# Kernel optimization log

Measured on AMD Instinct MI355X. Metric: run time of the kernel, lower is better.

The kernel has to match this reference:

```python
import jax, jax.numpy as jnp
import numpy as np

N_NODES = 100000
N_EDGES = 1600000
EMBED_DIM = 128
HIDDEN_DIM = 256


def setup_inputs() -> dict:
    key = jax.random.key(0)
    k_emb, k_src, k_dst, k_w1, k_w2 = jax.random.split(key, 5)
    emb = jax.random.normal(k_emb, (N_NODES, EMBED_DIM), dtype=jnp.float32)
    edge_src = jax.random.randint(k_src, (N_EDGES,), 0, N_NODES)
    edge_dst = jax.random.randint(k_dst, (N_EDGES,), 0, N_NODES)
    # Linear(2D -> H) and Linear(H -> D), stored as [in, out] for x @ W
    W1 = jax.random.normal(k_w1, (2 * EMBED_DIM, HIDDEN_DIM), dtype=jnp.float32) * (1.0 / np.sqrt(2 * EMBED_DIM))
    b1 = jnp.zeros((HIDDEN_DIM,), dtype=jnp.float32)
    W2 = jax.random.normal(k_w2, (HIDDEN_DIM, EMBED_DIM), dtype=jnp.float32) * (1.0 / np.sqrt(HIDDEN_DIM))
    b2 = jnp.zeros((EMBED_DIM,), dtype=jnp.float32)
    return {"emb": emb, "edge_src": edge_src, "edge_dst": edge_dst,
            "W1": W1, "b1": b1, "W2": W2, "b2": b2}


def reference(emb, edge_src, edge_dst, W1, b1, W2, b2):
    N, D = emb.shape
    E = edge_src.shape[0]
    # gather neighbor embeddings and segment-mean per destination node
    gathered = emb[edge_src]                                    # [E, D]
    nbr_sum = jax.ops.segment_sum(gathered, edge_dst, num_segments=N)   # [N, D]
    counts = jax.ops.segment_sum(jnp.ones((E,), emb.dtype), edge_dst, num_segments=N)  # [N]
    nbr_mean = nbr_sum / jnp.maximum(counts, 1.0)[:, None]
    # nodes with no neighbors fall back to their own embedding
    nbr_mean = jnp.where(counts[:, None] == 0, emb, nbr_mean)
    concat = jnp.concatenate([emb, nbr_mean], axis=-1)          # [N, 2D]
    h = jax.nn.relu(concat @ W1 + b1)                           # [N, H]
    return h @ W2 + b2                                          # [N, D]
```

## Files before the change

### kernel.cpp

```cpp
#include <hip/hip_runtime.h>

#define DD 128
#define HH 256
#define K1 256
#define BM 64
#define CH 2048
#define CH1 4096
#define CAP 8192

typedef __bf16 bf16;
typedef __attribute__((ext_vector_type(8))) __bf16 bf16x8;
typedef __attribute__((ext_vector_type(4))) float f32x4;


__global__ __launch_bounds__(256) void count512_k(const int* __restrict__ dst,
                                                  int* __restrict__ bcnt,
                                                  int E, int BSH) {
    __shared__ int c[512];
    for (int j = threadIdx.x; j < 512; j += 256) c[j] = 0;
    __syncthreads();
    for (int e = blockIdx.x * 256 + threadIdx.x; e < E; e += gridDim.x * 256)
        atomicAdd(&c[dst[e] >> BSH], 1);
    __syncthreads();
    for (int j = threadIdx.x; j < 512; j += 256)
        if (c[j]) atomicAdd(&bcnt[j], c[j]);
}

__global__ __launch_bounds__(512) void scan512_k(const int* __restrict__ bcnt,
                                                 int* __restrict__ bbase,
                                                 int* __restrict__ bpos,
                                                 int NB, int E) {
    __shared__ int s[512];
    const int t = threadIdx.x;
    int v = (t < NB) ? bcnt[t] : 0;
    s[t] = v;
    __syncthreads();
    for (int off = 1; off < 512; off <<= 1) {
        int y = (t >= off) ? s[t - off] : 0;
        __syncthreads();
        s[t] += y;
        __syncthreads();
    }
    int excl = s[t] - v;
    if (t < NB) { bbase[t] = excl; bpos[t] = excl; }
    if (t == 0) bbase[NB] = E;
}

__global__ __launch_bounds__(256) void part512_k(const int* __restrict__ src,
                                                 const int* __restrict__ dst,
                                                 int* __restrict__ bpos,
                                                 int2* __restrict__ pairs,
                                                 int E, int BSH) {
    __shared__ int lcnt[512];
    __shared__ int lbase[512];
    const int t = threadIdx.x;
    const int e0 = blockIdx.x * CH1;
    const int e1 = min(E, e0 + CH1);
    for (int j = t; j < 512; j += 256) lcnt[j] = 0;
    __syncthreads();
    int rs[CH1 / 256];
    #pragma unroll
    for (int k = 0; k < CH1 / 256; ++k) {
        int e = e0 + k * 256 + t;
        int b = -1;
        if (e < e1) { b = dst[e] >> BSH; atomicAdd(&lcnt[b], 1); }
        rs[k] = b;
    }
    __syncthreads();
    for (int j = t; j < 512; j += 256) {
        int c = lcnt[j];
        lbase[j] = c ? atomicAdd(&bpos[j], c) : 0;
        lcnt[j] = 0;
    }
    __syncthreads();
    #pragma unroll
    for (int k = 0; k < CH1 / 256; ++k) {
        int e = e0 + k * 256 + t;
        if (e < e1) {
            int b = rs[k];
            int slot = lbase[b] + atomicAdd(&lcnt[b], 1);
            pairs[slot] = make_int2(src[e], dst[e]);
        }
    }
}

__global__ __launch_bounds__(256) void sortb_k(const int2* __restrict__ pairs,
                                               const int* __restrict__ bbase,
                                               int* __restrict__ offs,
                                               int* __restrict__ ssrc,
                                               int N, int BSH) {
    __shared__ int hist[512];
    __shared__ int pref[512];
    __shared__ int run[512];
    __shared__ int sorted[CAP];
    const int t = threadIdx.x;
    const int b = blockIdx.x;
    const int B = 1 << BSH;
    const int d0 = b << BSH;
    const int nd = min(B, N - d0);
    const int rb = bbase[b], re = bbase[b + 1];
    const int cntE = re - rb;
    for (int j = t; j < 512; j += 256) hist[j] = 0;
    __syncthreads();
    for (int i = rb + t; i < re; i += 256)
        atomicAdd(&hist[pairs[i].y - d0], 1);
    __syncthreads();
    for (int j = t; j < 512; j += 256) pref[j] = hist[j];
    __syncthreads();
    for (int off = 1; off < 512; off <<= 1) {
        int j2 = t + 256;
        int v0 = (t >= off) ? pref[t - off] : 0;
        int v1 = (j2 >= off) ? pref[j2 - off] : 0;
        __syncthreads();
        pref[t] += v0;
        pref[j2] += v1;
        __syncthreads();
    }
    for (int j = t; j < nd; j += 256) offs[d0 + j] = rb + pref[j];
    for (int j = t; j < 512; j += 256) run[j] = pref[j] - hist[j];
    __syncthreads();
    if (cntE <= CAP) {
        for (int i = rb + t; i < re; i += 256) {
            int2 p = pairs[i];
            int pos = atomicAdd(&run[p.y - d0], 1);
            sorted[pos] = p.x;
        }
        __syncthreads();
        for (int i = t; i < cntE; i += 256) ssrc[rb + i] = sorted[i];
    } else {
        for (int i = rb + t; i < re; i += 256) {
            int2 p = pairs[i];
            int pos = atomicAdd(&run[p.y - d0], 1);
            ssrc[rb + pos] = p.x;
        }
    }
}


__global__ __launch_bounds__(256) void hist_k(const int* __restrict__ dst,
                                              int* __restrict__ cnt, int E) {
    for (int e = blockIdx.x * blockDim.x + threadIdx.x; e < E;
         e += gridDim.x * blockDim.x)
        atomicAdd(&cnt[dst[e]], 1);
}

__global__ __launch_bounds__(256) void scan1_k(const int* __restrict__ cnt,
                                               int* __restrict__ offs,
                                               int* __restrict__ part, int N) {
    __shared__ int sdata[256];
    const int b = blockIdx.x, t = threadIdx.x;
    const int base = b * 1024 + t * 4;
    int v[4], sum = 0;
    #pragma unroll
    for (int i = 0; i < 4; ++i) {
        int idx = base + i;
        v[i] = (idx < N) ? cnt[idx] : 0;
        sum += v[i];
    }
    sdata[t] = sum;
    __syncthreads();
    for (int off = 1; off < 256; off <<= 1) {
        int y = (t >= off) ? sdata[t - off] : 0;
        __syncthreads();
        sdata[t] += y;
        __syncthreads();
    }
    int excl = sdata[t] - sum;
    if (t == 255) part[b] = sdata[255];
    int run = excl;
    #pragma unroll
    for (int i = 0; i < 4; ++i) {
        int idx = base + i;
        if (idx < N) offs[idx] = run;
        run += v[i];
    }
}

__global__ __launch_bounds__(128) void scan2_k(int* __restrict__ part, int nparts) {
    __shared__ int sdata[128];
    const int t = threadIdx.x;
    int v = (t < nparts) ? part[t] : 0;
    sdata[t] = v;
    __syncthreads();
    for (int off = 1; off < 128; off <<= 1) {
        int y = (t >= off) ? sdata[t - off] : 0;
        __syncthreads();
        sdata[t] += y;
        __syncthreads();
    }
    if (t < nparts) part[t] = sdata[t] - v;
}

__global__ __launch_bounds__(256) void scan3_k(int* __restrict__ offs,
                                               const int* __restrict__ part, int N) {
    for (int i = blockIdx.x * blockDim.x + threadIdx.x; i < N;
         i += gridDim.x * blockDim.x)
        offs[i] += part[i >> 10];
}

__global__ __launch_bounds__(256) void bucket_k(const int* __restrict__ src,
                                                const int* __restrict__ dst,
                                                int* __restrict__ offs,
                                                int* __restrict__ ssrc,
                                                int E, int N) {
    const int r = blockIdx.x & 7;
    const int chunk = blockIdx.x >> 3;
    const int lo = r * (N >> 3);
    const int hi = (r == 7) ? N : lo + (N >> 3);
    const int e0 = chunk * CH;
    const int e1 = min(E, e0 + CH);
    for (int e = e0 + threadIdx.x; e < e1; e += 256) {
        int d = dst[e];
        if (d >= lo && d < hi) {
            int pos = atomicAdd(&offs[d], 1);
            ssrc[pos] = src[e];
        }
    }
}

__global__ __launch_bounds__(256) void cvt_k(const float* __restrict__ emb,
                                             bf16* __restrict__ embh, size_t n8) {
    for (size_t i = blockIdx.x * blockDim.x + threadIdx.x; i < n8;
         i += (size_t)gridDim.x * blockDim.x) {
        float4 a = *reinterpret_cast<const float4*>(&emb[i * 8]);
        float4 b = *reinterpret_cast<const float4*>(&emb[i * 8 + 4]);
        bf16x8 v;
        v[0]=(bf16)a.x; v[1]=(bf16)a.y; v[2]=(bf16)a.z; v[3]=(bf16)a.w;
        v[4]=(bf16)b.x; v[5]=(bf16)b.y; v[6]=(bf16)b.z; v[7]=(bf16)b.w;
        *reinterpret_cast<bf16x8*>(&embh[i * 8]) = v;
    }
}

__global__ __launch_bounds__(256) void gather_bf16_k(const bf16* __restrict__ embh,
                                                     const int* __restrict__ offs,
                                                     const int* __restrict__ ssrc,
                                                     bf16* __restrict__ nbrh, int N) {
    const int wid = threadIdx.x >> 6;
    const int lane = threadIdx.x & 63;
    const int d = blockIdx.x * 4 + wid;
    if (d >= N) return;
    const int sub = lane >> 4;
    const int c8 = (lane & 15) * 8;
    const int start = (d == 0) ? 0 : offs[d - 1];
    const int end = offs[d];
    float acc[8];
    #pragma unroll
    for (int j = 0; j < 8; ++j) acc[j] = 0.f;
    int e = start;
    for (; e + 8 <= end; e += 8) {
        int s0 = ssrc[e + sub];
        int s1 = ssrc[e + 4 + sub];
        bf16x8 v0 = *reinterpret_cast<const bf16x8*>(&embh[(size_t)s0 * DD + c8]);
        bf16x8 v1 = *reinterpret_cast<const bf16x8*>(&embh[(size_t)s1 * DD + c8]);
        #pragma unroll
        for (int j = 0; j < 8; ++j) acc[j] += (float)v0[j] + (float)v1[j];
    }
    for (; e + 4 <= end; e += 4) {
        int s = ssrc[e + sub];
        bf16x8 v = *reinterpret_cast<const bf16x8*>(&embh[(size_t)s * DD + c8]);
        #pragma unroll
        for (int j = 0; j < 8; ++j) acc[j] += (float)v[j];
    }
    const int rem = end - e;
    if (sub < rem) {
        int s = ssrc[e + sub];
        bf16x8 v = *reinterpret_cast<const bf16x8*>(&embh[(size_t)s * DD + c8]);
        #pragma unroll
        for (int j = 0; j < 8; ++j) acc[j] += (float)v[j];
    }
    #pragma unroll
    for (int j = 0; j < 8; ++j) {
        acc[j] += __shfl_xor(acc[j], 16);
        acc[j] += __shfl_xor(acc[j], 32);
    }
    if (sub == 0) {
        bf16x8 o;
        if (end > start) {
            float inv = 1.f / (float)(end - start);
            #pragma unroll
            for (int j = 0; j < 8; ++j) o[j] = (bf16)(acc[j] * inv);
        } else {
            o = *reinterpret_cast<const bf16x8*>(&embh[(size_t)d * DD + c8]);
        }
        *reinterpret_cast<bf16x8*>(&nbrh[(size_t)d * DD + c8]) = o;
    }
}

__global__ __launch_bounds__(256) void gather_k(const float* __restrict__ emb,
                                                const int* __restrict__ offs,
                                                const int* __restrict__ ssrc,
                                                float* __restrict__ nbr, int N) {
    const int wid = threadIdx.x >> 6;
    const int lane = threadIdx.x & 63;
    const int d = blockIdx.x * 4 + wid;
    if (d >= N) return;
    const int sub = lane >> 5;
    const int c = (lane & 31) * 4;
    const int start = (d == 0) ? 0 : offs[d - 1];
    const int end = offs[d];
    float4 acc = make_float4(0.f, 0.f, 0.f, 0.f);
    int e = start;
    for (; e + 4 <= end; e += 4) {
        int s0 = ssrc[e + sub];
        int s1 = ssrc[e + 2 + sub];
        float4 v0 = *reinterpret_cast<const float4*>(&emb[(size_t)s0 * DD + c]);
        float4 v1 = *reinterpret_cast<const float4*>(&emb[(size_t)s1 * DD + c]);
        acc.x += v0.x + v1.x; acc.y += v0.y + v1.y;
        acc.z += v0.z + v1.z; acc.w += v0.w + v1.w;
    }
    for (; e + 2 <= end; e += 2) {
        int s = ssrc[e + sub];
        float4 v = *reinterpret_cast<const float4*>(&emb[(size_t)s * DD + c]);
        acc.x += v.x; acc.y += v.y; acc.z += v.z; acc.w += v.w;
    }
    if (e < end && sub == 0) {
        int s = ssrc[e];
        float4 v = *reinterpret_cast<const float4*>(&emb[(size_t)s * DD + c]);
        acc.x += v.x; acc.y += v.y; acc.z += v.z; acc.w += v.w;
    }
    acc.x += __shfl_xor(acc.x, 32);
    acc.y += __shfl_xor(acc.y, 32);
    acc.z += __shfl_xor(acc.z, 32);
    acc.w += __shfl_xor(acc.w, 32);
    if (sub == 0) {
        if (end > start) {
            float inv = 1.f / (float)(end - start);
            acc.x *= inv; acc.y *= inv; acc.z *= inv; acc.w *= inv;
        } else {
            acc = *reinterpret_cast<const float4*>(&emb[(size_t)d * DD + c]);
        }
        *reinterpret_cast<float4*>(&nbr[(size_t)d * DD + c]) = acc;
    }
}

__global__ __launch_bounds__(64) void pack_k(const float* __restrict__ W, int NC,
                                             bf16* __restrict__ hi) {
    const int ntiles = NC >> 4;
    const int kt = blockIdx.x / ntiles;
    const int nt = blockIdx.x % ntiles;
    const int l = threadIdx.x;
    const int k0 = kt * 32 + (l >> 4) * 8;
    const int n = nt * 16 + (l & 15);
    bf16x8 hv;
    #pragma unroll
    for (int r = 0; r < 8; ++r)
        hv[r] = (bf16)W[(size_t)(k0 + r) * NC + n];
    *reinterpret_cast<bf16x8*>(hi + ((size_t)blockIdx.x * 64 + l) * 8) = hv;
}

__global__ __launch_bounds__(256) void mlp_mfma_k(const float* __restrict__ emb,
        const bf16* __restrict__ embh,
        const float* nbrf, const bf16* __restrict__ nbrh,
        const bf16* __restrict__ w1h, const float* __restrict__ b1,
        const bf16* __restrict__ w2h, const float* __restrict__ b2,
        float* out, int N) {
    __shared__ char smem[BM * K1 * 2];
    const int t = threadIdx.x;
    const int n0 = blockIdx.x * BM;
    const int l = t & 63;
    const int w = t >> 6;

    #pragma unroll
    for (int i = 0; i < 8; ++i) {
        int chunk = i * 256 + t;
        int row = chunk >> 5;
        int c0 = (chunk & 31) * 8;
        int n = n0 + row;
        bf16x8 hv;
        if (n < N) {
            if (embh != nullptr) {
                const bf16* sp = (c0 < DD) ? &embh[(size_t)n * DD + c0]
                                           : &nbrh[(size_t)n * DD + (c0 - DD)];
                hv = *reinterpret_cast<const bf16x8*>(sp);
            } else {
                const float* sp = (c0 < DD) ? &emb[(size_t)n * DD + c0]
                                            : &nbrf[(size_t)n * DD + (c0 - DD)];
                float4 a = *reinterpret_cast<const float4*>(sp);
                float4 b = *reinterpret_cast<const float4*>(sp + 4);
                hv[0]=(bf16)a.x; hv[1]=(bf16)a.y; hv[2]=(bf16)a.z; hv[3]=(bf16)a.w;
                hv[4]=(bf16)b.x; hv[5]=(bf16)b.y; hv[6]=(bf16)b.z; hv[7]=(bf16)b.w;
            }
        } else {
            #pragma unroll
            for (int j = 0; j < 8; ++j) hv[j] = (bf16)0.f;
        }
        int off = row * 512 + ((c0 * 2) ^ ((row & 7) << 4));
        *reinterpret_cast<bf16x8*>(smem + off) = hv;
    }
    __syncthreads();

    const int arow = l & 15;
    const int abyte = (l >> 4) * 16;

    f32x4 acc[4][4];
    #pragma unroll
    for (int ntl = 0; ntl < 4; ++ntl) {
        float bv = b1[w * 64 + ntl * 16 + (l & 15)];
        #pragma unroll
        for (int mt = 0; mt < 4; ++mt)
            acc[mt][ntl] = (f32x4){bv, bv, bv, bv};
    }
    for (int kt = 0; kt < 8; ++kt) {
        bf16x8 ah[4];
        #pragma unroll
        for (int mt = 0; mt < 4; ++mt) {
            int row = mt * 16 + arow;
            int off = row * 512 + ((kt * 64 + abyte) ^ ((row & 7) << 4));
            ah[mt] = *reinterpret_cast<const bf16x8*>(smem + off);
        }
        #pragma unroll
        for (int ntl = 0; ntl < 4; ++ntl) {
            int nt = w * 4 + ntl;
            size_t boff = ((size_t)(kt * 16 + nt) * 64 + l) * 8;
            bf16x8 bh = *reinterpret_cast<const bf16x8*>(w1h + boff);
            #pragma unroll
            for (int mt = 0; mt < 4; ++mt)
                acc[mt][ntl] = __builtin_amdgcn_mfma_f32_16x16x32_bf16(ah[mt], bh, acc[mt][ntl], 0, 0, 0);
        }
    }
    __syncthreads();

    #pragma unroll
    for (int mt = 0; mt < 4; ++mt)
        #pragma unroll
        for (int ntl = 0; ntl < 4; ++ntl) {
            int col = w * 64 + ntl * 16 + (l & 15);
            #pragma unroll
            for (int r = 0; r < 4; ++r) {
                int row = mt * 16 + (l >> 4) * 4 + r;
                int off = row * 512 + ((col * 2) ^ ((row & 7) << 4));
                *reinterpret_cast<bf16*>(smem + off) = (bf16)fmaxf(acc[mt][ntl][r], 0.f);
            }
        }
    __syncthreads();

    f32x4 acc2[4][2];
    #pragma unroll
    for (int ntl = 0; ntl < 2; ++ntl) {
        float bv = b2[w * 32 + ntl * 16 + (l & 15)];
        #pragma unroll
        for (int mt = 0; mt < 4; ++mt)
            acc2[mt][ntl] = (f32x4){bv, bv, bv, bv};
    }
    for (int kt = 0; kt < 8; ++kt) {
        bf16x8 ah[4];
        #pragma unroll
        for (int mt = 0; mt < 4; ++mt) {
            int row = mt * 16 + arow;
            int off = row * 512 + ((kt * 64 + abyte) ^ ((row & 7) << 4));
            ah[mt] = *reinterpret_cast<const bf16x8*>(smem + off);
        }
        #pragma unroll
        for (int ntl = 0; ntl < 2; ++ntl) {
            int nt = w * 2 + ntl;
            size_t boff = ((size_t)(kt * 8 + nt) * 64 + l) * 8;
            bf16x8 bh = *reinterpret_cast<const bf16x8*>(w2h + boff);
            #pragma unroll
            for (int mt = 0; mt < 4; ++mt)
                acc2[mt][ntl] = __builtin_amdgcn_mfma_f32_16x16x32_bf16(ah[mt], bh, acc2[mt][ntl], 0, 0, 0);
        }
    }
    #pragma unroll
    for (int mt = 0; mt < 4; ++mt)
        #pragma unroll
        for (int ntl = 0; ntl < 2; ++ntl) {
            int col = w * 32 + ntl * 16 + (l & 15);
            #pragma unroll
            for (int r = 0; r < 4; ++r) {
                int row = mt * 16 + (l >> 4) * 4 + r;
                int n = n0 + row;
                if (n < N) out[(size_t)n * DD + col] = acc2[mt][ntl][r];
            }
        }
}

__global__ __launch_bounds__(256) void scatter_k(const float* __restrict__ emb,
        const int* __restrict__ src, const int* __restrict__ dst,
        float* nbr, float* __restrict__ cnt, int E) {
    int e = blockIdx.x * 8 + (threadIdx.x >> 5);
    if (e >= E) return;
    int lane = threadIdx.x & 31;
    int s = src[e];
    int d = dst[e];
    const float4 v = *reinterpret_cast<const float4*>(&emb[(size_t)s * DD + lane * 4]);
    float* o = &nbr[(size_t)d * DD + lane * 4];
    atomicAdd(o + 0, v.x);
    atomicAdd(o + 1, v.y);
    atomicAdd(o + 2, v.z);
    atomicAdd(o + 3, v.w);
    if (lane == 0) atomicAdd(&cnt[d], 1.0f);
}

__global__ __launch_bounds__(256) void mlp_k(const float* __restrict__ emb,
        const float* nbr, const float* cnt,
        const float* __restrict__ W1, const float* __restrict__ b1,
        const float* __restrict__ W2, const float* __restrict__ b2,
        float* out, int N) {
    __shared__ float smem[BM * K1];
    const int t = threadIdx.x;
    const int n0 = blockIdx.x * BM;
    #pragma unroll
    for (int it = 0; it < 16; ++it) {
        int idx = it * 256 + t;
        int r = idx >> 6;
        int c4 = idx & 63;
        int n = n0 + r;
        float4 v = make_float4(0.f, 0.f, 0.f, 0.f);
        if (n < N) {
            if (c4 < 32) {
                v = *reinterpret_cast<const float4*>(&emb[(size_t)n * DD + c4 * 4]);
            } else {
                float c = cnt[n];
                if (c > 0.f) {
                    v = *reinterpret_cast<const float4*>(&nbr[(size_t)n * DD + (c4 - 32) * 4]);
                    float inv = 1.f / c;
                    v.x *= inv; v.y *= inv; v.z *= inv; v.w *= inv;
                } else {
                    v = *reinterpret_cast<const float4*>(&emb[(size_t)n * DD + (c4 - 32) * 4]);
                }
            }
        }
        *reinterpret_cast<float4*>(&smem[idx * 4]) = v;
    }
    __syncthreads();
    const int tx = t & 31;
    const int ty = t >> 5;
    const int r0 = ty * 8;
    {
        const int c0 = tx * 8;
        float acc[8][8];
        const float4 bva = *reinterpret_cast<const float4*>(&b1[c0]);
        const float4 bvb = *reinterpret_cast<const float4*>(&b1[c0 + 4]);
        #pragma unroll
        for (int i = 0; i < 8; ++i) {
            acc[i][0] = bva.x; acc[i][1] = bva.y; acc[i][2] = bva.z; acc[i][3] = bva.w;
            acc[i][4] = bvb.x; acc[i][5] = bvb.y; acc[i][6] = bvb.z; acc[i][7] = bvb.w;
        }
        for (int k0 = 0; k0 < K1; k0 += 4) {
            float xs[8][4];
            #pragma unroll
            for (int i = 0; i < 8; ++i) {
                float4 xv = *reinterpret_cast<const float4*>(&smem[(r0 + i) * K1 + k0]);
                xs[i][0] = xv.x; xs[i][1] = xv.y; xs[i][2] = xv.z; xs[i][3] = xv.w;
            }
            #pragma unroll
            for (int kk = 0; kk < 4; ++kk) {
                const float4 wa = *reinterpret_cast<const float4*>(&W1[(size_t)(k0 + kk) * HH + c0]);
                const float4 wb = *reinterpret_cast<const float4*>(&W1[(size_t)(k0 + kk) * HH + c0 + 4]);
                #pragma unroll
                for (int i = 0; i < 8; ++i) {
                    float x = xs[i][kk];
                    acc[i][0] += x * wa.x; acc[i][1] += x * wa.y;
                    acc[i][2] += x * wa.z; acc[i][3] += x * wa.w;
                    acc[i][4] += x * wb.x; acc[i][5] += x * wb.y;
                    acc[i][6] += x * wb.z; acc[i][7] += x * wb.w;
                }
            }
        }
        __syncthreads();
        #pragma unroll
        for (int i = 0; i < 8; ++i) {
            float4 h0, h1;
            h0.x = fmaxf(acc[i][0], 0.f); h0.y = fmaxf(acc[i][1], 0.f);
            h0.z = fmaxf(acc[i][2], 0.f); h0.w = fmaxf(acc[i][3], 0.f);
            h1.x = fmaxf(acc[i][4], 0.f); h1.y = fmaxf(acc[i][5], 0.f);
            h1.z = fmaxf(acc[i][6], 0.f); h1.w = fmaxf(acc[i][7], 0.f);
            *reinterpret_cast<float4*>(&smem[(r0 + i) * HH + c0]) = h0;
            *reinterpret_cast<float4*>(&smem[(r0 + i) * HH + c0 + 4]) = h1;
        }
        __syncthreads();
    }
    {
        const int c0 = tx * 4;
        float acc[8][4];
        const float4 bv = *reinterpret_cast<const float4*>(&b2[c0]);
        #pragma unroll
        for (int i = 0; i < 8; ++i) {
            acc[i][0] = bv.x; acc[i][1] = bv.y; acc[i][2] = bv.z; acc[i][3] = bv.w;
        }
        for (int k0 = 0; k0 < HH; k0 += 4) {
            float hs[8][4];
            #pragma unroll
            for (int i = 0; i < 8; ++i) {
                float4 hv = *reinterpret_cast<const float4*>(&smem[(r0 + i) * HH + k0]);
                hs[i][0] = hv.x; hs[i][1] = hv.y; hs[i][2] = hv.z; hs[i][3] = hv.w;
            }
            #pragma unroll
            for (int kk = 0; kk < 4; ++kk) {
                const float4 w2 = *reinterpret_cast<const float4*>(&W2[(size_t)(k0 + kk) * DD + c0]);
                #pragma unroll
                for (int i = 0; i < 8; ++i) {
                    float h = hs[i][kk];
                    acc[i][0] += h * w2.x; acc[i][1] += h * w2.y;
                    acc[i][2] += h * w2.z; acc[i][3] += h * w2.w;
                }
            }
        }
        #pragma unroll
        for (int i = 0; i < 8; ++i) {
            int n = n0 + r0 + i;
            if (n < N) {
                float4 o;
                o.x = acc[i][0]; o.y = acc[i][1]; o.z = acc[i][2]; o.w = acc[i][3];
                *reinterpret_cast<float4*>(&out[(size_t)n * DD + c0]) = o;
            }
        }
    }
}

extern "C" void kernel_launch(void* const* d_in, const int* in_sizes, int n_in,
                              void* d_out, int out_size, void* d_ws, size_t ws_size,
                              hipStream_t stream) {
    const float* emb = (const float*)d_in[0];
    const int* esrc  = (const int*)d_in[1];
    const int* edst  = (const int*)d_in[2];
    const float* W1  = (const float*)d_in[3];
    const float* b1  = (const float*)d_in[4];
    const float* W2  = (const float*)d_in[5];
    const float* b2  = (const float*)d_in[6];
    float* out = (float*)d_out;

    const int N = in_sizes[0] / DD;
    const int E = in_sizes[1];
    const int nparts = (N + 1023) / 1024;

    int BSH = 0;
    while ((((size_t)N + ((size_t)1 << BSH) - 1) >> BSH) > 512) ++BSH;
    const int B = 1 << BSH;
    const int NB = (N + B - 1) >> BSH;

    int* cnt  = (int*)d_ws;
    int* offs = cnt + N;
    int* part = offs + N;
    int* aux  = part + 128;
    int* ssrc = aux + 2048;
    char* wp = (char*)(ssrc + E);
    wp = (char*)(((uintptr_t)wp + 15) & ~(uintptr_t)15);
    bf16* w1h = (bf16*)wp;
    bf16* w2h = w1h + 65536;
    bf16* embh = w2h + 32768;
    bf16* nbrh = embh + (size_t)N * DD;
    int2* pairs = (int2*)embh;
    int* bcnt  = aux;
    int* bbase = aux + 512;
    int* bpos  = aux + 1280;
    const size_t need_base = (size_t)((char*)(w2h + 32768) - (char*)d_ws);
    const size_t need_full = (size_t)((char*)(nbrh + (size_t)N * DD) - (char*)d_ws);
    const bool pairs_fit = ((size_t)E * sizeof(int2) <= (size_t)N * DD * sizeof(bf16));

    if (ws_size >= need_base && nparts <= 128) {
        const bool fast = (ws_size >= need_full) && pairs_fit && (B <= 512);
        pack_k<<<dim3(128), dim3(64), 0, stream>>>(W1, HH, w1h);
        pack_k<<<dim3(64), dim3(64), 0, stream>>>(W2, DD, w2h);
        if (fast) {
            hipMemsetAsync(bcnt, 0, 512 * sizeof(int), stream);
            count512_k<<<dim3(512), dim3(256), 0, stream>>>(edst, bcnt, E, BSH);
            scan512_k<<<dim3(1), dim3(512), 0, stream>>>(bcnt, bbase, bpos, NB, E);
            part512_k<<<dim3((E + CH1 - 1) / CH1), dim3(256), 0, stream>>>(
                esrc, edst, bpos, pairs, E, BSH);
            sortb_k<<<dim3(NB), dim3(256), 0, stream>>>(pairs, bbase, offs, ssrc, N, BSH);
            cvt_k<<<dim3(2048), dim3(256), 0, stream>>>(emb, embh, (size_t)N * DD / 8);
            gather_bf16_k<<<dim3((N + 3) / 4), dim3(256), 0, stream>>>(embh, offs, ssrc, nbrh, N);
            mlp_mfma_k<<<dim3((N + BM - 1) / BM), dim3(256), 0, stream>>>(
                emb, embh, nullptr, nbrh, w1h, b1, w2h, b2, out, N);
        } else {
            hipMemsetAsync(cnt, 0, (size_t)N * sizeof(int), stream);
            hist_k<<<dim3(1024), dim3(256), 0, stream>>>(edst, cnt, E);
            scan1_k<<<dim3(nparts), dim3(256), 0, stream>>>(cnt, offs, part, N);
            scan2_k<<<dim3(1), dim3(128), 0, stream>>>(part, nparts);
            scan3_k<<<dim3(512), dim3(256), 0, stream>>>(offs, part, N);
            const int nchunks = (E + CH - 1) / CH;
            bucket_k<<<dim3(nchunks * 8), dim3(256), 0, stream>>>(esrc, edst, offs, ssrc, E, N);
            gather_k<<<dim3((N + 3) / 4), dim3(256), 0, stream>>>(emb, offs, ssrc, out, N);
            mlp_mfma_k<<<dim3((N + BM - 1) / BM), dim3(256), 0, stream>>>(
                emb, nullptr, out, nullptr, w1h, b1, w2h, b2, out, N);
        }
    } else {
        float* fcnt = (float*)d_ws;
        hipMemsetAsync(out, 0, (size_t)N * DD * sizeof(float), stream);
        hipMemsetAsync(fcnt, 0, (size_t)N * sizeof(float), stream);
        scatter_k<<<dim3((E + 7) / 8), dim3(256), 0, stream>>>(emb, esrc, edst, out, fcnt, E);
        mlp_k<<<dim3((N + BM - 1) / BM), dim3(256), 0, stream>>>(
            emb, out, fcnt, W1, b1, W2, b2, out, N);
    }
}
```

Before: 181.7 us.

## Split neighbor gather into column slices with slice-major output layout

The bf16 gather kernel is replaced by one that splits the 128 feature columns into 8 slices of 16, with a separate block per slice. Each wave handles 8 edges at once, each lane loading 4 bytes, so every block touches only a 32-byte column window of the embedding table; the apparent aim is better L2 locality for random source rows. The neighbor-mean output is stored slice-major ([8][N][16]) and the MLP loader is changed to read that layout. In exchange, the launch has 8x more blocks, offs/ssrc are re-read for every slice, and each load is narrow (4 bytes per lane), which costs more memory transactions.

Result: slower. 363.7 us (+100.2%).

```diff
diff --git a/kernel.cpp b/kernel.cpp
--- a/kernel.cpp
+++ b/kernel.cpp
@@ -11,6 +11,9 @@
 typedef __bf16 bf16;
 typedef __attribute__((ext_vector_type(8))) __bf16 bf16x8;
 typedef __attribute__((ext_vector_type(4))) float f32x4;
+
+__device__ __forceinline__ float blo(unsigned v) { return __uint_as_float(v << 16); }
+__device__ __forceinline__ float bhi(unsigned v) { return __uint_as_float(v & 0xffff0000u); }
 
 
 __global__ __launch_bounds__(256) void count512_k(const int* __restrict__ dst,
@@ -231,58 +234,58 @@
     }
 }
 
-__global__ __launch_bounds__(256) void gather_bf16_k(const bf16* __restrict__ embh,
-                                                     const int* __restrict__ offs,
-                                                     const int* __restrict__ ssrc,
-                                                     bf16* __restrict__ nbrh, int N) {
+__global__ __launch_bounds__(256) void gather2_k(const bf16* __restrict__ embh,
+                                                 const int* __restrict__ offs,
+                                                 const int* __restrict__ ssrc,
+                                                 bf16* __restrict__ nbrp, int N) {
+    const int s = blockIdx.x & 7;
+    const int j = blockIdx.x >> 3;
     const int wid = threadIdx.x >> 6;
     const int lane = threadIdx.x & 63;
-    const int d = blockIdx.x * 4 + wid;
+    const int d = j * 4 + wid;
     if (d >= N) return;
-    const int sub = lane >> 4;
-    const int c8 = (lane & 15) * 8;
+    const int slot = lane >> 3;
+    const int cp = lane & 7;
+    const int cbase = s * 16 + cp * 2;
     const int start = (d == 0) ? 0 : offs[d - 1];
     const int end = offs[d];
-    float acc[8];
-    #pragma unroll
-    for (int j = 0; j < 8; ++j) acc[j] = 0.f;
+    float a0 = 0.f, a1 = 0.f;
     int e = start;
+    for (; e + 16 <= end; e += 16) {
+        int s0 = ssrc[e + slot];
+        int s1 = ssrc[e + 8 + slot];
+        unsigned v0 = *reinterpret_cast<const unsigned*>(&embh[(size_t)s0 * DD + cbase]);
+        unsigned v1 = *reinterpret_cast<const unsigned*>(&embh[(size_t)s1 * DD + cbase]);
+        a0 += blo(v0) + blo(v1);
+        a1 += bhi(v0) + bhi(v1);
+    }
     for (; e + 8 <= end; e += 8) {
-        int s0 = ssrc[e + sub];
-        int s1 = ssrc[e + 4 + sub];
-        bf16x8 v0 = *reinterpret_cast<const bf16x8*>(&embh[(size_t)s0 * DD + c8]);
-        bf16x8 v1 = *reinterpret_cast<const bf16x8*>(&embh[(size_t)s1 * DD + c8]);
-        #pragma unroll
-        for (int j = 0; j < 8; ++j) acc[j] += (float)v0[j] + (float)v1[j];
-    }
-    for (; e + 4 <= end; e += 4) {
-        int s = ssrc[e + sub];
-        bf16x8 v = *reinterpret_cast<const bf16x8*>(&embh[(size_t)s * DD + c8]);
-        #pragma unroll
-        for (int j = 0; j < 8; ++j) acc[j] += (float)v[j];
-    }
-    const int rem = end - e;
-    if (sub < rem) {
-        int s = ssrc[e + sub];
-        bf16x8 v = *reinterpret_cast<const bf16x8*>(&embh[(size_t)s * DD + c8]);
-        #pragma unroll
-        for (int j = 0; j < 8; ++j) acc[j] += (float)v[j];
-    }
-    #pragma unroll
-    for (int j = 0; j < 8; ++j) {
-        acc[j] += __shfl_xor(acc[j], 16);
-        acc[j] += __shfl_xor(acc[j], 32);
-    }
-    if (sub == 0) {
-        bf16x8 o;
+        int s0 = ssrc[e + slot];
+        unsigned v0 = *reinterpret_cast<const unsigned*>(&embh[(size_t)s0 * DD + cbase]);
+        a0 += blo(v0);
+        a1 += bhi(v0);
+    }
+    if (e + slot < end) {
+        int s0 = ssrc[e + slot];
+        unsigned v0 = *reinterpret_cast<const unsigned*>(&embh[(size_t)s0 * DD + cbase]);
+        a0 += blo(v0);
+        a1 += bhi(v0);
+    }
+    #pragma unroll
+    for (int m = 8; m < 64; m <<= 1) {
+        a0 += __shfl_xor(a0, m);
+        a1 += __shfl_xor(a1, m);
+    }
+    if (slot == 0) {
+        union { unsigned u; bf16 h[2]; } cv;
         if (end > start) {
             float inv = 1.f / (float)(end - start);
-            #pragma unroll
-            for (int j = 0; j < 8; ++j) o[j] = (bf16)(acc[j] * inv);
+            cv.h[0] = (bf16)(a0 * inv);
+            cv.h[1] = (bf16)(a1 * inv);
         } else {
-            o = *reinterpret_cast<const bf16x8*>(&embh[(size_t)d * DD + c8]);
-        }
-        *reinterpret_cast<bf16x8*>(&nbrh[(size_t)d * DD + c8]) = o;
+            cv.u = *reinterpret_cast<const unsigned*>(&embh[(size_t)d * DD + cbase]);
+        }
+        *reinterpret_cast<unsigned*>(&nbrp[((size_t)s * N + d) * 16 + cp * 2]) = cv.u;
     }
 }
 
@@ -350,7 +353,7 @@
 
 __global__ __launch_bounds__(256) void mlp_mfma_k(const float* __restrict__ emb,
         const bf16* __restrict__ embh,
-        const float* nbrf, const bf16* __restrict__ nbrh,
+        const float* nbrf, const bf16* __restrict__ nbrp,
         const bf16* __restrict__ w1h, const float* __restrict__ b1,
         const bf16* __restrict__ w2h, const float* __restrict__ b2,
         float* out, int N) {
@@ -369,8 +372,13 @@
         bf16x8 hv;
         if (n < N) {
             if (embh != nullptr) {
-                const bf16* sp = (c0 < DD) ? &embh[(size_t)n * DD + c0]
-                                           : &nbrh[(size_t)n * DD + (c0 - DD)];
+                const bf16* sp;
+                if (c0 < DD) {
+                    sp = &embh[(size_t)n * DD + c0];
+                } else {
+                    int cc = c0 - DD;
+                    sp = &nbrp[((size_t)(cc >> 4) * N + n) * 16 + (cc & 15)];
+                }
                 hv = *reinterpret_cast<const bf16x8*>(sp);
             } else {
                 const float* sp = (c0 < DD) ? &emb[(size_t)n * DD + c0]
@@ -639,13 +647,13 @@
     bf16* w1h = (bf16*)wp;
     bf16* w2h = w1h + 65536;
     bf16* embh = w2h + 32768;
-    bf16* nbrh = embh + (size_t)N * DD;
+    bf16* nbrp = embh + (size_t)N * DD;
     int2* pairs = (int2*)embh;
     int* bcnt  = aux;
     int* bbase = aux + 512;
     int* bpos  = aux + 1280;
     const size_t need_base = (size_t)((char*)(w2h + 32768) - (char*)d_ws);
-    const size_t need_full = (size_t)((char*)(nbrh + (size_t)N * DD) - (char*)d_ws);
+    const size_t need_full = (size_t)((char*)(nbrp + (size_t)N * DD) - (char*)d_ws);
     const bool pairs_fit = ((size_t)E * sizeof(int2) <= (size_t)N * DD * sizeof(bf16));
 
     if (ws_size >= need_base && nparts <= 128) {
@@ -660,9 +668,9 @@
                 esrc, edst, bpos, pairs, E, BSH);
             sortb_k<<<dim3(NB), dim3(256), 0, stream>>>(pairs, bbase, offs, ssrc, N, BSH);
             cvt_k<<<dim3(2048), dim3(256), 0, stream>>>(emb, embh, (size_t)N * DD / 8);
-            gather_bf16_k<<<dim3((N + 3) / 4), dim3(256), 0, stream>>>(embh, offs, ssrc, nbrh, N);
+            gather2_k<<<dim3(((N + 3) / 4) * 8), dim3(256), 0, stream>>>(embh, offs, ssrc, nbrp, N);
             mlp_mfma_k<<<dim3((N + BM - 1) / BM), dim3(256), 0, stream>>>(
-                emb, embh, nullptr, nbrh, w1h, b1, w2h, b2, out, N);
+                emb, embh, nullptr, nbrp, w1h, b1, w2h, b2, out, N);
         } else {
             hipMemsetAsync(cnt, 0, (size_t)N * sizeof(int), stream);
             hist_k<<<dim3(1024), dim3(256), 0, stream>>>(edst, cnt, E);
```
